# Kernel optimization log

Measured on AMD Instinct MI355X. Metric: run time of the kernel, lower is better.

The kernel has to match this reference:

```python
import jax, jax.numpy as jnp
import numpy as np

N, DIM = 8192, 128

def setup_inputs() -> dict:
    key = jax.random.key(0)
    k1, k2, k3 = jax.random.split(key, 3)
    latent = jax.random.normal(k1, (N, DIM), dtype=jnp.float32)
    coords = jax.random.normal(k2, (N, 3), dtype=jnp.float32) * 5.0  # protein-scale spread
    alpha = jax.random.uniform(k3, (N,), dtype=jnp.float32)  # valid exponent range
    return {"latent": latent, "coords": coords, "alpha": alpha}

def _pairwise_dist(coords):
    # Euclidean cdist without materializing [N,N,3]
    sq = jnp.sum(coords * coords, axis=-1)  # [N]
    d2 = sq[:, None] + sq[None, :] - 2.0 * (coords @ coords.T)  # [N,N]
    return jnp.sqrt(jnp.maximum(d2, 1e-12))

def reference(latent, coords, alpha):
    D = _pairwise_dist(coords) + 1e-6  # [N,N]
    a = 0.5 * (alpha[:, None] + alpha[None, :])  # [N,N]
    # torch.no_grad() block -> stop_gradient on the clamped distance base
    D_safe = jax.lax.stop_gradient(jnp.clip(D, 1e-6, None))
    K = jnp.clip(D_safe ** (-a), 1e-8, 1000.0) * jnp.exp(-D / 12.0)
    K = jnp.clip(K, 0.0, 1000.0)
    n = K.shape[0]
    K = K * (1.0 - jnp.eye(n, dtype=K.dtype))  # fill_diagonal_(0)
    K = K / (jnp.sum(K, axis=-1, keepdims=True) + 1e-8)  # row-normalize
    out = K @ latent  # [N,DIM] aggregation
    return out, K
```

## Files before the change

kernel.cpp:

```cpp
#include <hip/hip_runtime.h>
#include <hip/hip_bf16.h>

constexpr int kN = 8192;
constexpr int kD = 128;
constexpr int BM = 32;
constexpr int BK = 64;
constexpr int JSPLIT = 8;
constexpr int LDB = 72;
constexpr int TB = 64;
constexpr int NB = kN / TB;

typedef __bf16 v8bf __attribute__((ext_vector_type(8)));
typedef float  v4f  __attribute__((ext_vector_type(4)));

__device__ __forceinline__ float kraw_f(float4 ci, float sqi, float4 cj, float sqj) {
    float d2 = sqi + sqj - 2.0f * (ci.x * cj.x + ci.y * cj.y + ci.z * cj.z);
    d2 = fmaxf(d2, 1e-12f);
    float Dd = __builtin_amdgcn_sqrtf(d2);
    float a = 0.5f * (ci.w + cj.w);
    float t = a * (-0.5f * __builtin_amdgcn_logf(d2));
    t = fminf(fmaxf(t, -26.575424759098897f), 9.965784284662087f);
    float K = __builtin_amdgcn_exp2f(fmaf(Dd, -0.12022458674074695f, t));
    return fminf(K, 1000.0f);
}

__global__ void pack_k(const float* __restrict__ coords, const float* __restrict__ alpha,
                       float4* __restrict__ c4, float* __restrict__ rsum) {
    int j = blockIdx.x * 256 + threadIdx.x;
    if (j < kN) {
        c4[j] = make_float4(coords[3 * j], coords[3 * j + 1], coords[3 * j + 2], alpha[j]);
        rsum[j] = 0.0f;
    }
}

__global__ __launch_bounds__(256) void fragprep_k(const float* __restrict__ latent,
                                                  __bf16* __restrict__ latTf,
                                                  float* __restrict__ outp) {
    __shared__ float ltile[32][132];
    const int jw = blockIdx.x;
    const int t = threadIdx.x;

    #pragma unroll
    for (int it = 0; it < 4; ++it) {
        int idx = it * 256 + t;
        int row = idx >> 5;
        int col = (idx & 31) * 4;
        float4 v = *reinterpret_cast<const float4*>(
            latent + (size_t)(jw * 32 + row) * kD + col);
        *reinterpret_cast<float4*>(&ltile[row][col]) = v;
    }

    {
        size_t base = ((size_t)jw * 256 + t) * 16;
        v4f z = {0.f, 0.f, 0.f, 0.f};
        #pragma unroll
        for (int e = 0; e < 4; ++e)
            *reinterpret_cast<v4f*>(outp + base + e * 4) = z;
    }
    __syncthreads();

    #pragma unroll
    for (int ss = 0; ss < 2; ++ss) {
        int s = ss * 256 + t;
        int d = s >> 6, l = s & 63;
        int jr = (l >> 4) * 8, dim = d * 16 + (l & 15);
        unsigned w[4];
        #pragma unroll
        for (int e2 = 0; e2 < 4; ++e2) {
            __bf16 lo = (__bf16)ltile[jr + 2 * e2][dim];
            __bf16 hi = (__bf16)ltile[jr + 2 * e2 + 1][dim];
            w[e2] = ((unsigned)*(unsigned short*)&hi << 16) | *(unsigned short*)&lo;
        }
        uint4 out = {w[0], w[1], w[2], w[3]};
        *reinterpret_cast<uint4*>((char*)latTf + (((size_t)jw * 8 + d) * 64 + l) * 16) = out;
    }
}

__global__ __launch_bounds__(256) void rowsum_sym_k(const float4* __restrict__ c4,
                                                    float* __restrict__ rsum) {
    __shared__ float4 rc4[TB];
    __shared__ float  rsq[TB];
    __shared__ float  rowbuf[TB][TB + 1];

    int L = blockIdx.x;
    int bi = (int)((2 * NB + 1 - sqrtf((float)((2 * NB + 1) * (2 * NB + 1) - 8 * L))) * 0.5f);
    #pragma unroll
    for (int f = 0; f < 2; ++f) {
        int s0 = bi * NB - bi * (bi - 1) / 2;
        int s1 = (bi + 1) * NB - (bi + 1) * bi / 2;
        if (L >= s1) ++bi;
        else if (L < s0) --bi;
    }
    int sbi = bi * NB - bi * (bi - 1) / 2;
    int bj = bi + (L - sbi);
    bool diag = (bi == bj);

    const int t = threadIdx.x;
    const int l = t & 63;
    const int w = t >> 6;

    if (t < TB) {
        float4 ci = c4[bi * TB + t];
        rc4[t] = ci;
        rsq[t] = ci.x * ci.x + ci.y * ci.y + ci.z * ci.z;
    }
    __syncthreads();

    float4 cj = c4[bj * TB + l];
    float sqj = cj.x * cj.x + cj.y * cj.y + cj.z * cj.z;

    float colacc = 0.f;
    #pragma unroll
    for (int rr = 0; rr < 16; ++rr) {
        int r = w * 16 + rr;
        float k = kraw_f(rc4[r], rsq[r], cj, sqj);
        if (diag && r == l) k = 0.f;
        colacc += k;
        rowbuf[r][l] = k;
    }
    __syncthreads();

    {
        int r = t >> 2, q = t & 3;
        float p = 0.f;
        #pragma unroll
        for (int m = 0; m < 16; ++m) p += rowbuf[r][q * 16 + m];
        p += __shfl_xor(p, 1, 64);
        p += __shfl_xor(p, 2, 64);
        if (q == 0) atomicAdd(&rsum[bi * TB + r], p);
    }
    if (!diag) atomicAdd(&rsum[bj * TB + l], colacc);
}

__global__ __launch_bounds__(256, 2) void main_k(
    const float4* __restrict__ c4, const float* __restrict__ rsum,
    const __bf16* __restrict__ latTf, float* __restrict__ outp, float* __restrict__ Kout) {

    __shared__ __bf16 Alds[BM][LDB];
    __shared__ float4 c4row[BM];
    __shared__ float  sqrow[BM];
    __shared__ float  invrow[BM];

    const int t = threadIdx.x;
    const int i0 = blockIdx.x * BM;
    const int jstrip = blockIdx.y * (kN / JSPLIT);

    if (t < BM) {
        float4 ci = c4[i0 + t];
        c4row[t] = ci;
        sqrow[t] = ci.x * ci.x + ci.y * ci.y + ci.z * ci.z;
        invrow[t] = 1.0f / (rsum[i0 + t] + 1e-8f);
    }
    __syncthreads();

    const int lane = t & 63;
    const int wave = t >> 6;

    const int c2 = t & 31;
    const int rb = (t >> 5) * 4;

    float4 rc[4]; float rs[4], rv[4];
    #pragma unroll
    for (int rr = 0; rr < 4; ++rr) {
        rc[rr] = c4row[rb + rr];
        rs[rr] = sqrow[rb + rr];
        rv[rr] = invrow[rb + rr];
    }

    const int arow = lane & 15;
    const int koff = (lane >> 4) * 8;
    const char* bfb = (const char*)latTf + (size_t)lane * 16;

    v4f acc[2][2];
    #pragma unroll
    for (int rt = 0; rt < 2; ++rt)
        #pragma unroll
        for (int dt = 0; dt < 2; ++dt) acc[rt][dt] = (v4f){0.f, 0.f, 0.f, 0.f};

    for (int cb = 0; cb < kN / JSPLIT / BK; ++cb) {
        const int j0 = jstrip + cb * BK;

        const int gjA = j0 + 2 * c2, gjB = gjA + 1;
        const float4 cjA = c4[gjA];
        const float4 cjB = c4[gjB];
        const float sqA = cjA.x * cjA.x + cjA.y * cjA.y + cjA.z * cjA.z;
        const float sqB = cjB.x * cjB.x + cjB.y * cjB.y + cjB.z * cjB.z;
        #pragma unroll
        for (int rr = 0; rr < 4; ++rr) {
            int r = rb + rr, gi = i0 + r;
            float kA = (gi == gjA) ? 0.0f : kraw_f(rc[rr], rs[rr], cjA, sqA);
            float kB = (gi == gjB) ? 0.0f : kraw_f(rc[rr], rs[rr], cjB, sqB);
            float knA = kA * rv[rr];
            float knB = kB * rv[rr];
            float2 st = {knA, knB};
            *reinterpret_cast<float2*>(Kout + (size_t)gi * kN + gjA) = st;
            __bf16 hA = (__bf16)knA, hB = (__bf16)knB;
            unsigned pk = ((unsigned)*(unsigned short*)&hB << 16) | *(unsigned short*)&hA;
            *reinterpret_cast<unsigned*>(&Alds[r][2 * c2]) = pk;
        }
        __syncthreads();

        #pragma unroll
        for (int kk = 0; kk < 2; ++kk) {
            const size_t jw = (size_t)(j0 >> 5) + kk;
            v8bf a0 = *reinterpret_cast<const v8bf*>(&Alds[arow][kk * 32 + koff]);
            v8bf a1 = *reinterpret_cast<const v8bf*>(&Alds[16 + arow][kk * 32 + koff]);
            v8bf b0 = *reinterpret_cast<const v8bf*>(bfb + (jw * 8 + wave * 2)     * 1024);
            v8bf b1 = *reinterpret_cast<const v8bf*>(bfb + (jw * 8 + wave * 2 + 1) * 1024);
            acc[0][0] = __builtin_amdgcn_mfma_f32_16x16x32_bf16(a0, b0, acc[0][0], 0, 0, 0);
            acc[0][1] = __builtin_amdgcn_mfma_f32_16x16x32_bf16(a0, b1, acc[0][1], 0, 0, 0);
            acc[1][0] = __builtin_amdgcn_mfma_f32_16x16x32_bf16(a1, b0, acc[1][0], 0, 0, 0);
            acc[1][1] = __builtin_amdgcn_mfma_f32_16x16x32_bf16(a1, b1, acc[1][1], 0, 0, 0);
        }
        __syncthreads();
    }

    const int row = (lane >> 4) * 4;
    const int col0 = wave * 32 + (lane & 15);
    #pragma unroll
    for (int rt = 0; rt < 2; ++rt)
        #pragma unroll
        for (int dt = 0; dt < 2; ++dt)
            #pragma unroll
            for (int q = 0; q < 4; ++q)
                atomicAdd(&outp[(size_t)(i0 + rt * 16 + row + q) * kD + col0 + dt * 16],
                          acc[rt][dt][q]);
}

extern "C" void kernel_launch(void* const* d_in, const int* in_sizes, int n_in,
                              void* d_out, int out_size, void* d_ws, size_t ws_size,
                              hipStream_t stream) {
    const float* latent = (const float*)d_in[0];
    const float* coords = (const float*)d_in[1];
    const float* alpha  = (const float*)d_in[2];

    float* outp = (float*)d_out;
    float* Kout = (float*)d_out + (size_t)kN * kD;

    char* ws = (char*)d_ws;
    __bf16* latTf = (__bf16*)ws;
    float4* c4    = (float4*)(ws + 2u * 1024 * 1024);
    float*  rsum  = (float*)(ws + 2u * 1024 * 1024 + 128 * 1024);

    pack_k<<<dim3(kN / 256), dim3(256), 0, stream>>>(coords, alpha, c4, rsum);
    fragprep_k<<<dim3(kN / 32), dim3(256), 0, stream>>>(latent, latTf, outp);
    rowsum_sym_k<<<dim3(NB * (NB + 1) / 2), dim3(256), 0, stream>>>(c4, rsum);
    main_k<<<dim3(kN / BM, JSPLIT), dim3(256), 0, stream>>>(c4, rsum, latTf, outp, Kout);
}
```

Measured before the change: 118.5 us.

## Split fused K-compute/GEMM into separate K-write and GEMM kernels

Unfuses the main kernel into two. The first computes the normalized kernel matrix and writes it with 16-byte vector stores. The second reads K back from global memory, converts it to bf16 and runs the MFMA aggregation. The intent is to get wider stores and to stop the transcendental math from stalling the matrix pipeline, but it adds a full read of the 256MB K matrix and an extra launch.

```diff
diff --git a/kernel.cpp b/kernel.cpp
--- a/kernel.cpp
+++ b/kernel.cpp
@@ -6,6 +6,7 @@
 constexpr int BM = 32;
 constexpr int BK = 64;
 constexpr int JSPLIT = 8;
+constexpr int KJS = 8;
 constexpr int LDB = 72;
 constexpr int TB = 64;
 constexpr int NB = kN / TB;
@@ -132,40 +133,59 @@
     if (!diag) atomicAdd(&rsum[bj * TB + l], colacc);
 }
 
-__global__ __launch_bounds__(256, 2) void main_k(
+__global__ __launch_bounds__(256) void kwrite_k(
     const float4* __restrict__ c4, const float* __restrict__ rsum,
-    const __bf16* __restrict__ latTf, float* __restrict__ outp, float* __restrict__ Kout) {
+    float* __restrict__ Kout) {
+
+    const int t = threadIdx.x;
+    const int lane = t & 63;
+    const int wave = t >> 6;
+    const int i0 = blockIdx.x * 16;
+    const int gi = i0 + (lane & 15);
+    const int koff = (lane >> 4) * 8;
+
+    const float4 ci = c4[gi];
+    const float sqi = ci.x * ci.x + ci.y * ci.y + ci.z * ci.z;
+    const float inv_i = 1.0f / (rsum[gi] + 1e-8f);
+
+    const int jbase = blockIdx.y * (kN / KJS) + wave * (kN / KJS / 4);
+    constexpr int NIT = kN / KJS / 4 / 32;
+
+    for (int cb = 0; cb < NIT; ++cb) {
+        const int jc = jbase + cb * 32 + koff;
+
+        float kn[8];
+        #pragma unroll
+        for (int e = 0; e < 8; ++e) {
+            float4 cj = c4[jc + e];
+            float sqj = cj.x * cj.x + cj.y * cj.y + cj.z * cj.z;
+            float k = (gi == jc + e) ? 0.0f : kraw_f(ci, sqi, cj, sqj);
+            kn[e] = k * inv_i;
+        }
+
+        float* kp = Kout + (size_t)gi * kN + jc;
+        v4f s0 = {kn[0], kn[1], kn[2], kn[3]};
+        v4f s1 = {kn[4], kn[5], kn[6], kn[7]};
+        *reinterpret_cast<v4f*>(kp)     = s0;
+        *reinterpret_cast<v4f*>(kp + 4) = s1;
+    }
+}
+
+__global__ __launch_bounds__(256, 2) void gemm_k(
+    const float* __restrict__ Kin, const __bf16* __restrict__ latTf,
+    float* __restrict__ outp) {
 
     __shared__ __bf16 Alds[BM][LDB];
-    __shared__ float4 c4row[BM];
-    __shared__ float  sqrow[BM];
-    __shared__ float  invrow[BM];
 
     const int t = threadIdx.x;
     const int i0 = blockIdx.x * BM;
     const int jstrip = blockIdx.y * (kN / JSPLIT);
 
-    if (t < BM) {
-        float4 ci = c4[i0 + t];
-        c4row[t] = ci;
-        sqrow[t] = ci.x * ci.x + ci.y * ci.y + ci.z * ci.z;
-        invrow[t] = 1.0f / (rsum[i0 + t] + 1e-8f);
-    }
-    __syncthreads();
-
     const int lane = t & 63;
     const int wave = t >> 6;
 
     const int c2 = t & 31;
     const int rb = (t >> 5) * 4;
-
-    float4 rc[4]; float rs[4], rv[4];
-    #pragma unroll
-    for (int rr = 0; rr < 4; ++rr) {
-        rc[rr] = c4row[rb + rr];
-        rs[rr] = sqrow[rb + rr];
-        rv[rr] = invrow[rb + rr];
-    }
 
     const int arow = lane & 15;
     const int koff = (lane >> 4) * 8;
@@ -179,22 +199,13 @@
 
     for (int cb = 0; cb < kN / JSPLIT / BK; ++cb) {
         const int j0 = jstrip + cb * BK;
-
-        const int gjA = j0 + 2 * c2, gjB = gjA + 1;
-        const float4 cjA = c4[gjA];
-        const float4 cjB = c4[gjB];
-        const float sqA = cjA.x * cjA.x + cjA.y * cjA.y + cjA.z * cjA.z;
-        const float sqB = cjB.x * cjB.x + cjB.y * cjB.y + cjB.z * cjB.z;
+        const int gjA = j0 + 2 * c2;
+
         #pragma unroll
         for (int rr = 0; rr < 4; ++rr) {
             int r = rb + rr, gi = i0 + r;
-            float kA = (gi == gjA) ? 0.0f : kraw_f(rc[rr], rs[rr], cjA, sqA);
-            float kB = (gi == gjB) ? 0.0f : kraw_f(rc[rr], rs[rr], cjB, sqB);
-            float knA = kA * rv[rr];
-            float knB = kB * rv[rr];
-            float2 st = {knA, knB};
-            *reinterpret_cast<float2*>(Kout + (size_t)gi * kN + gjA) = st;
-            __bf16 hA = (__bf16)knA, hB = (__bf16)knB;
+            float2 kn = *reinterpret_cast<const float2*>(Kin + (size_t)gi * kN + gjA);
+            __bf16 hA = (__bf16)kn.x, hB = (__bf16)kn.y;
             unsigned pk = ((unsigned)*(unsigned short*)&hB << 16) | *(unsigned short*)&hA;
             *reinterpret_cast<unsigned*>(&Alds[r][2 * c2]) = pk;
         }
@@ -245,5 +256,6 @@
     pack_k<<<dim3(kN / 256), dim3(256), 0, stream>>>(coords, alpha, c4, rsum);
     fragprep_k<<<dim3(kN / 32), dim3(256), 0, stream>>>(latent, latTf, outp);
     rowsum_sym_k<<<dim3(NB * (NB + 1) / 2), dim3(256), 0, stream>>>(c4, rsum);
-    main_k<<<dim3(kN / BM, JSPLIT), dim3(256), 0, stream>>>(c4, rsum, latTf, outp, Kout);
-}
+    kwrite_k<<<dim3(kN / 16, KJS), dim3(256), 0, stream>>>(c4, rsum, Kout);
+    gemm_k<<<dim3(kN / BM, JSPLIT), dim3(256), 0, stream>>>(Kout, latTf, outp);
+}
```

New measurement: 202.8 us. 71.1% more time.
